# Optimization experiments

Hardware: AMD Instinct MI355X
Metric: run time of the kernel (lower is better)

The kernel has to match this reference:

```python
import jax, jax.numpy as jnp
import numpy as np
import math

# Config constants (match init_kwargs)
E = 8          # n_experts
TOPK = 2       # attn_topk
DIM = 1024     # transformer_dim
B = 4          # batch_size
S = 1024       # max_seq_len
H = 1024       # num_heads * head_dim
SCALE = 1.0 / math.sqrt(DIM)  # original divides scores by sqrt(self.dim)


def setup_inputs() -> dict:
    key = jax.random.key(0)
    ks = jax.random.split(key, 8)
    w = 0.02  # weight init scale
    return {
        "X": jax.random.normal(ks[0], (B, S, DIM), jnp.float32),
        "mask": jnp.ones((B, S), jnp.float32),
        "switch_W": jax.random.normal(ks[1], (DIM * S, E), jnp.float32) * w,
        "switch_b": jnp.zeros((E,), jnp.float32),
        "Wq": jax.random.normal(ks[2], (E, DIM, H), jnp.float32) * w,
        "bq": jnp.zeros((E, H), jnp.float32),
        "Wk": jax.random.normal(ks[3], (E, DIM, H), jnp.float32) * w,
        "bk": jnp.zeros((E, H), jnp.float32),
        "Wv": jax.random.normal(ks[4], (E, DIM, H), jnp.float32) * w,
        "bv": jnp.zeros((E, H), jnp.float32),
        "Wff": jax.random.normal(ks[5], (E, H, DIM), jnp.float32) * w,
        "bff": jnp.zeros((E, DIM), jnp.float32),
    }


def _dispatch_mask(route_prob):
    # top-k expert routing per batch element -> hard {0,1} mask [B, E]
    _, idx = jax.lax.top_k(route_prob, TOPK)  # [B, TOPK]
    b = route_prob.shape[0]
    return jnp.zeros((b, E), route_prob.dtype).at[jnp.arange(b)[:, None], idx].set(1.0)


def reference(X, mask, switch_W, switch_b, Wq, bq, Wk, bk, Wv, bv, Wff, bff):
    b, s, d = X.shape
    # Router: Linear(dim*seq_len -> n_experts) + softmax; preprocess -> idx_list
    logits = X.reshape(b, -1) @ switch_W + switch_b          # [B, E]
    route_prob = jax.nn.softmax(logits, axis=-1)
    m = _dispatch_mask(route_prob)                            # [B, E] dispatch mask (idx_list)

    # Per-expert Q/K/V projections (ColumnParallelLinearWithMoE over routed batches)
    Q = jnp.einsum('bsd,edh->ebsh', X, Wq) + bq[:, None, None, :]  # [E,B,S,H]
    K = jnp.einsum('bsd,edh->ebsh', X, Wk) + bk[:, None, None, :]
    V = jnp.einsum('bsd,edh->ebsh', X, Wv) + bv[:, None, None, :]

    # RowParallelMatmulWithMoE: per-expert scores, softmax (dropout p=0)
    scores = jnp.einsum('ebsh,ebth->ebst', Q, K) * SCALE      # [E,B,S,S]
    P = jax.nn.softmax(scores, axis=-1)

    # index_add_ combine of per-expert attn maps (second preprocess reuses same routing)
    A = jnp.einsum('be,ebst->bst', m, P)                      # [B,S,S]

    # ColumnParallelMatmulWithMoE: attn @ V per expert
    ctx = jnp.einsum('bst,ebth->ebsh', A, V)                  # [E,B,S,H]

    # RowParallelLinearWithMoE output projection, then index_add_ combine
    out = jnp.einsum('ebsh,ehd->ebsd', ctx, Wff) + bff[:, None, None, :]
    y = jnp.einsum('be,ebsd->bsd', m, out)                    # [B,S,DIM]
    return y
```

## Files before the change

### kernel.cpp

```cpp
#include <hip/hip_runtime.h>
#include <math.h>

typedef unsigned short u16;
typedef __attribute__((ext_vector_type(8))) short bffrag;
typedef __attribute__((ext_vector_type(4))) float f32x4;
typedef __attribute__((ext_vector_type(4))) unsigned short us4;
typedef __attribute__((ext_vector_type(8))) unsigned short us8;

#define SCALE_QK (1.0f/32.0f)

__device__ __forceinline__ u16 f2bf(float f) {
    unsigned u = __builtin_bit_cast(unsigned, f);
    u += 0x7fffu + ((u >> 16) & 1u);
    return (u16)(u >> 16);
}
__device__ __forceinline__ float bf2f(u16 v) {
    unsigned u = ((unsigned)v) << 16;
    return __builtin_bit_cast(float, u);
}

__device__ __forceinline__ void gld16(const u16* g, u16* l) {
    __builtin_amdgcn_global_load_lds(
        (const __attribute__((address_space(1))) void*)g,
        (__attribute__((address_space(3))) void*)l, 16, 0, 0);
}

__global__ __launch_bounds__(256) void router_partial(const float* __restrict__ X,
                                                      const float* __restrict__ sW,
                                                      float* __restrict__ part) {
    float acc[32];
    #pragma unroll
    for (int a = 0; a < 32; ++a) acc[a] = 0.f;
    int tid = blockIdx.x * 256 + threadIdx.x;
    #pragma unroll
    for (int q = 0; q < 4; ++q) {
        int i = tid + q * 262144;
        float4 w0 = *(const float4*)(sW + (size_t)i * 8);
        float4 w1 = *(const float4*)(sW + (size_t)i * 8 + 4);
        #pragma unroll
        for (int b = 0; b < 4; ++b) {
            float x = X[((size_t)b << 20) + i];
            acc[b*8+0] += x * w0.x; acc[b*8+1] += x * w0.y;
            acc[b*8+2] += x * w0.z; acc[b*8+3] += x * w0.w;
            acc[b*8+4] += x * w1.x; acc[b*8+5] += x * w1.y;
            acc[b*8+6] += x * w1.z; acc[b*8+7] += x * w1.w;
        }
    }
    __shared__ float wsum[4][32];
    int lane = threadIdx.x & 63, wv = threadIdx.x >> 6;
    #pragma unroll
    for (int a = 0; a < 32; ++a) {
        float v = acc[a];
        #pragma unroll
        for (int off = 32; off; off >>= 1) v += __shfl_down(v, off, 64);
        if (lane == 0) wsum[wv][a] = v;
    }
    __syncthreads();
    int t = threadIdx.x;
    if (t < 32)
        part[(size_t)t * 1024 + blockIdx.x] = wsum[0][t] + wsum[1][t] + wsum[2][t] + wsum[3][t];
}

__global__ __launch_bounds__(256) void router_final(const float* __restrict__ part,
                                                    const float* __restrict__ sb,
                                                    int* __restrict__ sel_need) {
    __shared__ float ps[32][8];
    __shared__ float lg[32];
    int t = threadIdx.x, a = t >> 3, c = t & 7;
    {
        float s = 0.f;
        const float* p = part + (size_t)a * 1024 + c * 128;
        for (int i = 0; i < 128; ++i) s += p[i];
        ps[a][c] = s;
    }
    __syncthreads();
    if (t < 32) {
        float v = 0.f;
        #pragma unroll
        for (int j = 0; j < 8; ++j) v += ps[t][j];
        lg[t] = v + sb[t & 7];
    }
    __syncthreads();
    if (t < 4) {
        int base = t * 8;
        int e1 = 0; float v1 = lg[base];
        for (int e = 1; e < 8; ++e) { if (lg[base + e] > v1) { v1 = lg[base + e]; e1 = e; } }
        int e2 = -1; float v2 = -INFINITY;
        for (int e = 0; e < 8; ++e) {
            if (e == e1) continue;
            if (lg[base + e] > v2) { v2 = lg[base + e]; e2 = e; }
        }
        sel_need[t * 2] = e1; sel_need[t * 2 + 1] = e2;
    }
    __syncthreads();
    if (t < 8) {
        int need = 0;
        for (int j = 0; j < 8; ++j) need |= (sel_need[j] == t);
        sel_need[8 + t] = need;
    }
}

__global__ __launch_bounds__(256) void c1_partial(const float* __restrict__ Wff,
        const float* __restrict__ bv, const int* __restrict__ sel_need,
        float* __restrict__ cpart) {
    int e = blockIdx.z;
    if (!sel_need[8 + e]) return;
    int d = blockIdx.x * 256 + threadIdx.x;
    int h0 = blockIdx.y * 128;
    const float* W = Wff + ((size_t)e << 20) + (size_t)h0 * 1024 + d;
    const float* bvp = bv + e * 1024 + h0;
    float s = 0.f;
    #pragma unroll 4
    for (int h = 0; h < 128; ++h) s += bvp[h] * W[(size_t)h * 1024];
    cpart[(e * 8 + blockIdx.y) * 1024 + d] = s;
}

__global__ __launch_bounds__(256) void cvt_all(const float* __restrict__ Wq,
                                               const float* __restrict__ Wk,
                                               const float* __restrict__ Wff,
                                               const float* __restrict__ X,
                                               const float* __restrict__ Wv,
                                               const int* __restrict__ sel_need,
                                               u16* __restrict__ WqT, u16* __restrict__ WkT,
                                               u16* __restrict__ WffT,
                                               u16* __restrict__ Xb, u16* __restrict__ WvB) {
    int z = blockIdx.z;
    int R0 = blockIdx.y * 128, C0 = blockIdx.x * 128;
    int t = threadIdx.x;
    if (z < 24) {
        int type = z >> 3, e = z & 7;
        if (!sel_need[8 + e]) return;
        const float* src = (type == 0 ? Wq : type == 1 ? Wk : Wff) + ((size_t)e << 20);
        u16* dst = (type == 0 ? WqT : type == 1 ? WkT : WffT) + ((size_t)e << 20);
        __shared__ u16 lt[128 * 136];
        int c = t & 127;
        int rh = (t >> 7) * 4;
        #pragma unroll
        for (int it = 0; it < 16; ++it) {
            int r4 = it * 8 + rh;
            us4 o;
            #pragma unroll
            for (int j = 0; j < 4; ++j)
                o[j] = f2bf(src[(size_t)(R0 + r4 + j) * 1024 + C0 + c]);
            *(us4*)&lt[c * 136 + r4] = o;
        }
        __syncthreads();
        int dd = (t & 15) * 8;
        int hh = t >> 4;
        #pragma unroll
        for (int it = 0; it < 8; ++it) {
            int cr = it * 16 + hh;
            us8 o = *(const us8*)&lt[cr * 136 + dd];
            *(us8*)(dst + (size_t)(C0 + cr) * 1024 + R0 + dd) = o;
        }
    } else {
        const float* src; u16* dst;
        if (z < 28) {
            int b = z - 24;
            src = X + ((size_t)b << 20);  dst = Xb + ((size_t)b << 20);
        } else {
            int e = z - 28;
            if (!sel_need[8 + e]) return;
            src = Wv + ((size_t)e << 20);  dst = WvB + ((size_t)e << 20);
        }
        int r = t >> 4;
        int c8 = (t & 15) * 8;
        #pragma unroll
        for (int it = 0; it < 8; ++it) {
            int row = R0 + it * 16 + r;
            const float* sp = src + (size_t)row * 1024 + C0 + c8;
            float4 a = *(const float4*)sp;
            float4 b2 = *(const float4*)(sp + 4);
            us8 o;
            o[0] = f2bf(a.x); o[1] = f2bf(a.y); o[2] = f2bf(a.z); o[3] = f2bf(a.w);
            o[4] = f2bf(b2.x); o[5] = f2bf(b2.y); o[6] = f2bf(b2.z); o[7] = f2bf(b2.w);
            *(us8*)(dst + (size_t)row * 1024 + C0 + c8) = o;
        }
    }
}

__device__ __forceinline__ void stage_half8(const u16* g, int ld, u16* ldst, int tid) {
    int r = tid >> 3;
    int j = ((tid ^ r) & 7) * 8;
    gld16(g + (size_t)r * ld + j, ldst + tid * 8);
    gld16(g + (size_t)(r + 64) * ld + j, ldst + 4096 + tid * 8);
}

template<int Q, bool LASTVM>
__device__ __forceinline__ void phase8(const u16* Ac, const bffrag (&bfr)[4][2],
                                       f32x4 (&acc)[8][4], int rb, int l15, int x0,
                                       const u16* sg, int sld, u16* sdst, int tid) {
    bffrag af[2][2];
    #pragma unroll
    for (int mm = 0; mm < 2; ++mm) {
        int r = (rb + Q * 32 + mm * 16 + l15) * 64;
        af[mm][0] = *(const bffrag*)(Ac + r + x0);
        af[mm][1] = *(const bffrag*)(Ac + r + (x0 ^ 32));
    }
    __builtin_amdgcn_sched_barrier(0);
    stage_half8(sg, sld, sdst, tid);
    __builtin_amdgcn_sched_barrier(0);
    __builtin_amdgcn_s_barrier();
    asm volatile("s_waitcnt lgkmcnt(0)" ::: "memory");
    __builtin_amdgcn_sched_barrier(0);
    __builtin_amdgcn_s_setprio(1);
    #pragma unroll
    for (int ks = 0; ks < 2; ++ks)
        #pragma unroll
        for (int mm = 0; mm < 2; ++mm)
            #pragma unroll
            for (int nn = 0; nn < 4; ++nn)
                acc[Q*2+mm][nn] = __builtin_amdgcn_mfma_f32_16x16x32_bf16(
                    af[mm][ks], bfr[nn][ks], acc[Q*2+mm][nn], 0, 0, 0);
    __builtin_amdgcn_s_setprio(0);
    __builtin_amdgcn_sched_barrier(0);
    if (LASTVM) asm volatile("s_waitcnt vmcnt(4)" ::: "memory");
    __builtin_amdgcn_s_barrier();
}

__device__ __forceinline__ void gemm8(const u16* __restrict__ A, int lda,
                                      const u16* __restrict__ B, int ldb,
                                      int K, int m0, int n0, f32x4 (&acc)[8][4]) {
    __shared__ u16 lds[65536];
    const int tid = threadIdx.x, l = tid & 63, wid = tid >> 6;
    const int wr = wid >> 2, wc = wid & 3;
    const int l15 = l & 15;
    const int rb = wr * 128;
    const int cb = wc * 64;
    const int x0 = (((l >> 4) ^ (l & 7)) * 8);
    const int nt = K >> 6;

    const u16* Ag = A + (size_t)m0 * lda;
    const u16* Bg = B + (size_t)n0 * ldb;

    stage_half8(Ag,                          lda, lds,                 tid);
    stage_half8(Ag + (size_t)128 * lda,      lda, lds + 8192,          tid);
    stage_half8(Bg,                          ldb, lds + 16384,         tid);
    stage_half8(Bg + (size_t)128 * ldb,      ldb, lds + 16384 + 8192,  tid);
    stage_half8(Bg + 64,                     ldb, lds + 32768 + 16384, tid);
    stage_half8(Bg + 64 + (size_t)128 * ldb, ldb, lds + 32768 + 16384 + 8192, tid);
    asm volatile("s_waitcnt vmcnt(4)" ::: "memory");
    __builtin_amdgcn_s_barrier();

    for (int t7 = 0; t7 < nt; ++t7) {
        const int cur = t7 & 1;
        u16* Ac = lds + cur * 32768;
        u16* Bc = Ac + 16384;
        u16* An = lds + (cur ^ 1) * 32768;
        const int ka = (t7 + 1 < nt ? t7 + 1 : nt - 1) << 6;
        const int kb = (t7 + 2 < nt ? t7 + 2 : nt - 1) << 6;
        const u16* sA0 = Ag + ka;
        const u16* sA1 = Ag + (size_t)128 * lda + ka;
        const u16* sB0 = Bg + kb;
        const u16* sB1 = Bg + (size_t)128 * ldb + kb;

        bffrag bfr[4][2];
        #pragma unroll
        for (int nn = 0; nn < 4; ++nn) {
            int r = (cb + nn * 16 + l15) * 64;
            bfr[nn][0] = *(const bffrag*)(Bc + r + x0);
            bfr[nn][1] = *(const bffrag*)(Bc + r + (x0 ^ 32));
        }
        phase8<0, false>(Ac, bfr, acc, rb, l15, x0, sA0, lda, An, tid);
        phase8<1, false>(Ac, bfr, acc, rb, l15, x0, sA1, lda, An + 8192, tid);
        phase8<2, false>(Ac, bfr, acc, rb, l15, x0, sB0, ldb, Bc, tid);
        phase8<3, true >(Ac, bfr, acc, rb, l15, x0, sB1, ldb, Bc + 8192, tid);
    }
}

__device__ __forceinline__ void zero8(f32x4 (&acc)[8][4]) {
    #pragma unroll
    for (int m = 0; m < 8; ++m)
        #pragma unroll
        for (int n = 0; n < 4; ++n)
            #pragma unroll
            for (int i = 0; i < 4; ++i) acc[m][n][i] = 0.f;
}

__device__ __forceinline__ void epi8_bf16(u16* __restrict__ C, int ldc, float scale,
                                          const f32x4 (&acc)[8][4],
                                          const float* __restrict__ biasN,
                                          int M0, int N0) {
    const int tid = threadIdx.x, l = tid & 63, wid = tid >> 6;
    const int wr = wid >> 2, wc = wid & 3;
    const int m0 = M0 + wr * 128, n0 = N0 + wc * 64;
    const int l15 = l & 15, l4 = (l >> 4) * 4;
    #pragma unroll
    for (int mt = 0; mt < 8; ++mt)
        #pragma unroll
        for (int nn = 0; nn < 4; ++nn) {
            int col = n0 + nn * 16 + l15;
            float bn = biasN ? biasN[col] : 0.f;
            #pragma unroll
            for (int i = 0; i < 4; ++i) {
                int row = m0 + mt * 16 + l4 + i;
                C[(size_t)row * ldc + col] = f2bf(acc[mt][nn][i] * scale + bn);
            }
        }
}

__device__ __forceinline__ void xcd_decode(int f, int& z, int& m0, int& n0) {
    int xcd = f & 7, slot = f >> 3;
    z = xcd + ((slot >> 4) << 3);
    int idx = slot & 15;
    m0 = (idx >> 2) * 256;
    n0 = (idx & 3) * 256;
}

__global__ __launch_bounds__(512) void mfma8_qk(const u16* __restrict__ Xb,
        const u16* __restrict__ WqT, const u16* __restrict__ WkT,
        const float* __restrict__ bq, const float* __restrict__ bk,
        const int* __restrict__ sel, u16* __restrict__ Qb, u16* __restrict__ Kb) {
    int z, m0, n0;
    xcd_decode(blockIdx.x, z, m0, n0);
    int w = z >> 3, bs = z & 7;
    int b = bs >> 1, e = sel[bs];
    f32x4 acc[8][4]; zero8(acc);
    gemm8(Xb + ((size_t)b << 20), 1024, (w ? WkT : WqT) + ((size_t)e << 20), 1024,
          1024, m0, n0, acc);
    epi8_bf16((w ? Kb : Qb) + ((size_t)bs << 20), 1024, 1.0f, acc,
              (w ? bk : bq) + e * 1024, m0, n0);
}

__global__ __launch_bounds__(512) void mfma8_sw(const u16* __restrict__ Qb,
        const u16* __restrict__ Kb, const u16* __restrict__ WffT,
        const u16* __restrict__ WvB, const int* __restrict__ sel,
        u16* __restrict__ Sb, u16* __restrict__ P0b, u16* __restrict__ P1b) {
    int z, m0, n0;
    xcd_decode(blockIdx.x, z, m0, n0);
    f32x4 acc[8][4]; zero8(acc);
    if (z < 8) {
        gemm8(Qb + ((size_t)z << 20), 1024, Kb + ((size_t)z << 20), 1024, 1024, m0, n0, acc);
        epi8_bf16(Sb + ((size_t)z << 20), 1024, SCALE_QK, acc, nullptr, m0, n0);
    } else {
        int h = (z >= 12), b = z & 3, e = sel[b * 2 + h];
        gemm8(WffT + ((size_t)e << 20), 1024, WvB + ((size_t)e << 20), 1024, 1024, m0, n0, acc);
        epi8_bf16((h ? P1b : P0b) + ((size_t)b << 20), 1024, 1.0f, acc, nullptr, m0, n0);
    }
}

__global__ __launch_bounds__(256) void wvfadd(const u16* __restrict__ P0b,
                                              const u16* __restrict__ P1b,
                                              u16* __restrict__ W,
                                              const float* __restrict__ cpart,
                                              const float* __restrict__ bff,
                                              const int* __restrict__ sel,
                                              float* __restrict__ ybias) {
    int bid = blockIdx.x;
    if (bid >= 2048) {
        int r = bid - 2048;
        int b = r >> 2;
        int d = (r & 3) * 256 + threadIdx.x;
        int e0 = sel[b * 2], e1 = sel[b * 2 + 1];
        float c0 = 0.f, c1v = 0.f;
        #pragma unroll
        for (int hc = 0; hc < 8; ++hc) {
            c0  += cpart[(e0 * 8 + hc) * 1024 + d];
            c1v += cpart[(e1 * 8 + hc) * 1024 + d];
        }
        ybias[b * 1024 + d] = 2.f * (c0 + c1v) + bff[e0 * 1024 + d] + bff[e1 * 1024 + d];
        return;
    }
    size_t i = (size_t)(bid * 256 + threadIdx.x) * 8;
    us8 a = *(const us8*)(P0b + i);
    us8 b = *(const us8*)(P1b + i);
    us8 o;
    #pragma unroll
    for (int j = 0; j < 8; ++j) o[j] = f2bf(bf2f(a[j]) + bf2f(b[j]));
    *(us8*)(W + i) = o;
}

__device__ __forceinline__ void stage_tile(const u16* a0, const u16* a1,
                                           const u16* b0, const u16* b1,
                                           u16* sa, u16* sb, int tid) {
    gld16(a0, &sa[tid * 8]);
    gld16(a1, &sa[2048 + tid * 8]);
    gld16(b0, &sb[tid * 8]);
    gld16(b1, &sb[2048 + tid * 8]);
}

__device__ __forceinline__ void gemm_ds(const u16* __restrict__ A, int lda,
                                        const u16* __restrict__ B, int ldb,
                                        int K, int m0, int n0, f32x4 (&acc)[4][4]) {
    __shared__ u16 sA[2][4096];
    __shared__ u16 sB[2][4096];
    const int tid = threadIdx.x, lane = tid & 63, wv = tid >> 6;
    const int wr = (wv >> 1) * 64, wc = (wv & 1) * 64;
    const int l15 = lane & 15, lk = (lane >> 4) * 8;
    const int r0 = tid >> 2, k8 = (tid & 3) * 8;

    const u16* a0 = A + (size_t)(m0 + r0) * lda + k8;
    const u16* a1 = A + (size_t)(m0 + 64 + r0) * lda + k8;
    const u16* b0 = B + (size_t)(n0 + r0) * ldb + k8;
    const u16* b1 = B + (size_t)(n0 + 64 + r0) * ldb + k8;

    stage_tile(a0, a1, b0, b1, sA[0], sB[0], tid);
    __syncthreads();

    const int nt = K >> 5;
    for (int t = 0; t < nt; ++t) {
        const int cur = t & 1;
        if (t + 1 < nt) {
            int k0 = (t + 1) << 5;
            stage_tile(a0 + k0, a1 + k0, b0 + k0, b1 + k0, sA[cur ^ 1], sB[cur ^ 1], tid);
        }
        bffrag av[4], bf[4];
        #pragma unroll
        for (int m = 0; m < 4; ++m)
            av[m] = *reinterpret_cast<const bffrag*>(&sA[cur][(wr + m * 16 + l15) * 32 + lk]);
        #pragma unroll
        for (int n = 0; n < 4; ++n)
            bf[n] = *reinterpret_cast<const bffrag*>(&sB[cur][(wc + n * 16 + l15) * 32 + lk]);
        #pragma unroll
        for (int m = 0; m < 4; ++m)
            #pragma unroll
            for (int n = 0; n < 4; ++n)
                acc[m][n] = __builtin_amdgcn_mfma_f32_16x16x32_bf16(av[m], bf[n], acc[m][n], 0, 0, 0);
        __syncthreads();
    }
}

__device__ __forceinline__ void zero_acc(f32x4 (&acc)[4][4]) {
    #pragma unroll
    for (int m = 0; m < 4; ++m)
        #pragma unroll
        for (int n = 0; n < 4; ++n)
            #pragma unroll
            for (int i = 0; i < 4; ++i) acc[m][n][i] = 0.f;
}

__device__ __forceinline__ void epi4_bf16(u16* __restrict__ C, int ldc, int m0, int n0,
                                          const f32x4 (&acc)[4][4]) {
    const int tid = threadIdx.x, lane = tid & 63, wv = tid >> 6;
    const int wr = (wv >> 1) * 64, wc = (wv & 1) * 64;
    const int l15 = lane & 15, l4 = (lane >> 4) * 4;
    #pragma unroll
    for (int m = 0; m < 4; ++m)
        #pragma unroll
        for (int n = 0; n < 4; ++n) {
            int col = n0 + wc + n * 16 + l15;
            #pragma unroll
            for (int i = 0; i < 4; ++i) {
                int row = m0 + wr + m * 16 + l4 + i;
                C[(size_t)row * ldc + col] = f2bf(acc[m][n][i]);
            }
        }
}

__device__ __forceinline__ void epi4_f32(float* __restrict__ C, int ldc, int m0, int n0,
                                         const f32x4 (&acc)[4][4],
                                         const float* __restrict__ bias1) {
    const int tid = threadIdx.x, lane = tid & 63, wv = tid >> 6;
    const int wr = (wv >> 1) * 64, wc = (wv & 1) * 64;
    const int l15 = lane & 15, l4 = (lane >> 4) * 4;
    #pragma unroll
    for (int m = 0; m < 4; ++m)
        #pragma unroll
        for (int n = 0; n < 4; ++n) {
            int col = n0 + wc + n * 16 + l15;
            float bn = bias1 ? bias1[col] : 0.f;
            #pragma unroll
            for (int i = 0; i < 4; ++i) {
                int row = m0 + wr + m * 16 + l4 + i;
                C[(size_t)row * ldc + col] = acc[m][n][i] + bn;
            }
        }
}

__global__ __launch_bounds__(256) void sm_mt(const u16* __restrict__ Sb, u16* __restrict__ Ab,
        const u16* __restrict__ Wvfsum, const u16* __restrict__ Xb, u16* __restrict__ Mtb) {
    int bid = blockIdx.x;
    if (bid < 256) {
        int b = bid >> 6, m0 = ((bid >> 3) & 7) * 128, n0 = (bid & 7) * 128;
        f32x4 acc[4][4]; zero_acc(acc);
        gemm_ds(Wvfsum + ((size_t)b << 20), 1024, Xb + ((size_t)b << 20), 1024, 1024, m0, n0, acc);
        epi4_bf16(Mtb + ((size_t)b << 20), 1024, m0, n0, acc);
        return;
    }
    int bs = bid - 256, b = bs >> 10, s = bs & 1023;
    const u16* S0 = Sb + ((size_t)(b * 2) << 20) + (size_t)s * 1024;
    const u16* S1 = S0 + (1u << 20);
    int t = threadIdx.x, lane = t & 63, wv = t >> 6;
    us4 xv0 = *(const us4*)(S0 + t * 4);
    us4 xv1 = *(const us4*)(S1 + t * 4);
    float x0[4], x1[4];
    #pragma unroll
    for (int j = 0; j < 4; ++j) { x0[j] = bf2f(xv0[j]); x1[j] = bf2f(xv1[j]); }
    float m0 = fmaxf(fmaxf(x0[0], x0[1]), fmaxf(x0[2], x0[3]));
    float m1 = fmaxf(fmaxf(x1[0], x1[1]), fmaxf(x1[2], x1[3]));
    #pragma unroll
    for (int off = 32; off; off >>= 1) {
        m0 = fmaxf(m0, __shfl_xor(m0, off, 64));
        m1 = fmaxf(m1, __shfl_xor(m1, off, 64));
    }
    __shared__ float wred[4][4];
    if (lane == 0) { wred[wv][0] = m0; wred[wv][1] = m1; }
    __syncthreads();
    m0 = fmaxf(fmaxf(wred[0][0], wred[1][0]), fmaxf(wred[2][0], wred[3][0]));
    m1 = fmaxf(fmaxf(wred[0][1], wred[1][1]), fmaxf(wred[2][1], wred[3][1]));
    float e0[4], e1[4];
    #pragma unroll
    for (int j = 0; j < 4; ++j) { e0[j] = __expf(x0[j] - m0); e1[j] = __expf(x1[j] - m1); }
    float s0 = e0[0] + e0[1] + e0[2] + e0[3];
    float s1 = e1[0] + e1[1] + e1[2] + e1[3];
    #pragma unroll
    for (int off = 32; off; off >>= 1) {
        s0 += __shfl_xor(s0, off, 64);
        s1 += __shfl_xor(s1, off, 64);
    }
    if (lane == 0) { wred[wv][2] = s0; wred[wv][3] = s1; }
    __syncthreads();
    s0 = wred[0][2] + wred[1][2] + wred[2][2] + wred[3][2];
    s1 = wred[0][3] + wred[1][3] + wred[2][3] + wred[3][3];
    float r0 = 1.f / s0, r1 = 1.f / s1;
    us4 o;
    #pragma unroll
    for (int j = 0; j < 4; ++j) o[j] = f2bf(e0[j] * r0 + e1[j] * r1);
    *(us4*)(Ab + ((size_t)b << 20) + (size_t)s * 1024 + t * 4) = o;
}

__global__ __launch_bounds__(256) void mfma_y(const u16* __restrict__ Abf,
        const u16* __restrict__ Mtb, const float* __restrict__ ybias,
        float* __restrict__ y) {
    int b = blockIdx.z;
    int m0 = blockIdx.y * 128, n0 = blockIdx.x * 128;
    f32x4 acc[4][4]; zero_acc(acc);
    gemm_ds(Abf + ((size_t)b << 20), 1024, Mtb + ((size_t)b << 20), 1024, 1024, m0, n0, acc);
    epi4_f32(y + ((size_t)b << 20), 1024, m0, n0, acc, ybias + b * 1024);
}

extern "C" void kernel_launch(void* const* d_in, const int* in_sizes, int n_in,
                              void* d_out, int out_size, void* d_ws, size_t ws_size,
                              hipStream_t stream) {
    const float* X   = (const float*)d_in[0];
    const float* sW  = (const float*)d_in[2];
    const float* sb  = (const float*)d_in[3];
    const float* Wq  = (const float*)d_in[4];
    const float* bq  = (const float*)d_in[5];
    const float* Wk  = (const float*)d_in[6];
    const float* bk  = (const float*)d_in[7];
    const float* Wv  = (const float*)d_in[8];
    const float* bv  = (const float*)d_in[9];
    const float* Wff = (const float*)d_in[10];
    const float* bff = (const float*)d_in[11];
    float* y = (float*)d_out;

    char* w = (char*)d_ws;
    float* part  = (float*)w;
    float* cpart = (float*)w;
    int*   sel   = (int*)(w + (1u << 18));
    float* ybias = (float*)(w + (1u << 18) + 256);
    u16* base = (u16*)(w + (1u << 19));
    u16* Xb   = base;
    u16* WqT  = Xb   + (4u << 20);
    u16* WkT  = WqT  + (8u << 20);
    u16* WffT = WkT  + (8u << 20);
    u16* WvB  = WffT + (8u << 20);
    u16* Qb   = WvB  + (8u << 20);
    u16* Kb   = Qb   + (8u << 20);
    u16* Sb   = Kb   + (8u << 20);
    u16* P0b  = Sb   + (8u << 20);
    u16* P1b  = P0b  + (4u << 20);
    u16* Abf    = WqT;
    u16* Mtb    = WkT;
    u16* Wvfsum = Qb;

    router_partial<<<1024, 256, 0, stream>>>(X, sW, part);
    router_final<<<1, 256, 0, stream>>>(part, sb, sel);
    c1_partial<<<dim3(4, 8, 8), 256, 0, stream>>>(Wff, bv, sel, cpart);
    cvt_all<<<dim3(8, 8, 36), 256, 0, stream>>>(Wq, Wk, Wff, X, Wv, sel,
                                                WqT, WkT, WffT, Xb, WvB);

    mfma8_qk<<<256, 512, 0, stream>>>(Xb, WqT, WkT, bq, bk, sel, Qb, Kb);
    mfma8_sw<<<256, 512, 0, stream>>>(Qb, Kb, WffT, WvB, sel, Sb, P0b, P1b);
    wvfadd<<<2064, 256, 0, stream>>>(P0b, P1b, Wvfsum, cpart, bff, sel, ybias);
    sm_mt<<<4352, 256, 0, stream>>>(Sb, Abf, Wvfsum, Xb, Mtb);
    mfma_y<<<dim3(8, 8, 4), 256, 0, stream>>>(Abf, Mtb, ybias, y);
}
```

Baseline: 213.9 us.

## Fuse bias-projection partials into router kernel and vectorize weight transpose loads

The per-expert bias projection (bv·Wff) partial sums now run inside the router partial kernel as 256 extra blocks, which removes one kernel launch and lets that work overlap with the router reduction. The cost is that all 8 experts are now computed unconditionally, because routing is not yet known at that point. The transposing bf16 conversion in cvt_all now reads rows with float4 loads and stores them into an XOR-swizzled LDS tile. It then gathers transposed columns element by element, replacing the earlier strided scalar global reads. The workspace offsets are adjusted so cpart no longer aliases part.

```diff
diff --git a/kernel.cpp b/kernel.cpp
--- a/kernel.cpp
+++ b/kernel.cpp
@@ -25,13 +25,31 @@
         (__attribute__((address_space(3))) void*)l, 16, 0, 0);
 }
 
-__global__ __launch_bounds__(256) void router_partial(const float* __restrict__ X,
-                                                      const float* __restrict__ sW,
-                                                      float* __restrict__ part) {
+__global__ __launch_bounds__(256) void router_c1(const float* __restrict__ X,
+                                                 const float* __restrict__ sW,
+                                                 float* __restrict__ part,
+                                                 const float* __restrict__ Wff,
+                                                 const float* __restrict__ bv,
+                                                 float* __restrict__ cpart) {
+    int bid = blockIdx.x;
+    if (bid < 256) {
+        int e = bid >> 5;
+        int r = bid & 31;
+        int d = (r & 3) * 256 + threadIdx.x;
+        int h0 = (r >> 2) * 128;
+        const float* W = Wff + ((size_t)e << 20) + (size_t)h0 * 1024 + d;
+        const float* bvp = bv + e * 1024 + h0;
+        float s = 0.f;
+        #pragma unroll 4
+        for (int h = 0; h < 128; ++h) s += bvp[h] * W[(size_t)h * 1024];
+        cpart[(e * 8 + (r >> 2)) * 1024 + d] = s;
+        return;
+    }
+    int rbid = bid - 256;
     float acc[32];
     #pragma unroll
     for (int a = 0; a < 32; ++a) acc[a] = 0.f;
-    int tid = blockIdx.x * 256 + threadIdx.x;
+    int tid = rbid * 256 + threadIdx.x;
     #pragma unroll
     for (int q = 0; q < 4; ++q) {
         int i = tid + q * 262144;
@@ -58,7 +76,7 @@
     __syncthreads();
     int t = threadIdx.x;
     if (t < 32)
-        part[(size_t)t * 1024 + blockIdx.x] = wsum[0][t] + wsum[1][t] + wsum[2][t] + wsum[3][t];
+        part[(size_t)t * 1024 + rbid] = wsum[0][t] + wsum[1][t] + wsum[2][t] + wsum[3][t];
 }
 
 __global__ __launch_bounds__(256) void router_final(const float* __restrict__ part,
@@ -98,21 +116,6 @@
         for (int j = 0; j < 8; ++j) need |= (sel_need[j] == t);
         sel_need[8 + t] = need;
     }
-}
-
-__global__ __launch_bounds__(256) void c1_partial(const float* __restrict__ Wff,
-        const float* __restrict__ bv, const int* __restrict__ sel_need,
-        float* __restrict__ cpart) {
-    int e = blockIdx.z;
-    if (!sel_need[8 + e]) return;
-    int d = blockIdx.x * 256 + threadIdx.x;
-    int h0 = blockIdx.y * 128;
-    const float* W = Wff + ((size_t)e << 20) + (size_t)h0 * 1024 + d;
-    const float* bvp = bv + e * 1024 + h0;
-    float s = 0.f;
-    #pragma unroll 4
-    for (int h = 0; h < 128; ++h) s += bvp[h] * W[(size_t)h * 1024];
-    cpart[(e * 8 + blockIdx.y) * 1024 + d] = s;
 }
 
 __global__ __launch_bounds__(256) void cvt_all(const float* __restrict__ Wq,
@@ -133,16 +136,19 @@
         const float* src = (type == 0 ? Wq : type == 1 ? Wk : Wff) + ((size_t)e << 20);
         u16* dst = (type == 0 ? WqT : type == 1 ? WkT : WffT) + ((size_t)e << 20);
         __shared__ u16 lt[128 * 136];
-        int c = t & 127;
-        int rh = (t >> 7) * 4;
-        #pragma unroll
-        for (int it = 0; it < 16; ++it) {
-            int r4 = it * 8 + rh;
-            us4 o;
-            #pragma unroll
-            for (int j = 0; j < 4; ++j)
-                o[j] = f2bf(src[(size_t)(R0 + r4 + j) * 1024 + C0 + c]);
-            *(us4*)&lt[c * 136 + r4] = o;
+        int r = t >> 4;
+        int c8 = (t & 15) * 8;
+        #pragma unroll
+        for (int it = 0; it < 8; ++it) {
+            int row = it * 16 + r;
+            const float* sp = src + (size_t)(R0 + row) * 1024 + C0 + c8;
+            float4 a = *(const float4*)sp;
+            float4 b2 = *(const float4*)(sp + 4);
+            us8 o;
+            o[0] = f2bf(a.x); o[1] = f2bf(a.y); o[2] = f2bf(a.z); o[3] = f2bf(a.w);
+            o[4] = f2bf(b2.x); o[5] = f2bf(b2.y); o[6] = f2bf(b2.z); o[7] = f2bf(b2.w);
+            int cs = c8 ^ (((row >> 3) & 7) << 3);
+            *(us8*)&lt[row * 136 + cs] = o;
         }
         __syncthreads();
         int dd = (t & 15) * 8;
@@ -150,7 +156,13 @@
         #pragma unroll
         for (int it = 0; it < 8; ++it) {
             int cr = it * 16 + hh;
-            us8 o = *(const us8*)&lt[cr * 136 + dd];
+            us8 o;
+            #pragma unroll
+            for (int j = 0; j < 8; ++j) {
+                int row = dd + j;
+                int cs = cr ^ (((row >> 3) & 7) << 3);
+                o[j] = lt[row * 136 + cs];
+            }
             *(us8*)(dst + (size_t)(C0 + cr) * 1024 + R0 + dd) = o;
         }
     } else {
@@ -547,9 +559,9 @@
 
     char* w = (char*)d_ws;
     float* part  = (float*)w;
-    float* cpart = (float*)w;
-    int*   sel   = (int*)(w + (1u << 18));
-    float* ybias = (float*)(w + (1u << 18) + 256);
+    float* cpart = (float*)(w + (1u << 17));
+    int*   sel   = (int*)(w + 393216);
+    float* ybias = (float*)(w + 393216 + 256);
     u16* base = (u16*)(w + (1u << 19));
     u16* Xb   = base;
     u16* WqT  = Xb   + (4u << 20);
@@ -565,9 +577,8 @@
     u16* Mtb    = WkT;
     u16* Wvfsum = Qb;
 
-    router_partial<<<1024, 256, 0, stream>>>(X, sW, part);
+    router_c1<<<1280, 256, 0, stream>>>(X, sW, part, Wff, bv, cpart);
     router_final<<<1, 256, 0, stream>>>(part, sb, sel);
-    c1_partial<<<dim3(4, 8, 8), 256, 0, stream>>>(Wff, bv, sel, cpart);
     cvt_all<<<dim3(8, 8, 36), 256, 0, stream>>>(Wq, Wk, Wff, X, Wv, sel,
                                                 WqT, WkT, WffT, Xb, WvB);
 
```

Measured after the change: 203.9 us, median of 3. 1.05x faster.
